# Optimization experiments

Measured on AMD Instinct MI355X. Metric: run time of the kernel, lower is better.

The kernel has to match this reference:

```python
import jax, jax.numpy as jnp
import numpy as np

N_NODES = 50000
N_EDGES = 1600000
N_FEATURES = 1433
HIDDEN = 256
N_CLASSES = 7


def setup_inputs() -> dict:
    key = jax.random.key(0)
    ks = jax.random.split(key, 5)
    x = jax.random.normal(ks[0], (N_NODES, N_FEATURES), dtype=jnp.float32)
    edge_index = jax.random.randint(ks[1], (2, N_EDGES), 0, N_NODES, dtype=jnp.int64)
    # Glorot-style init like PyG's Linear inside GCNConv
    W1 = jax.random.normal(ks[2], (N_FEATURES, HIDDEN), dtype=jnp.float32) * (1.0 / np.sqrt(N_FEATURES))
    b1 = jnp.zeros((HIDDEN,), dtype=jnp.float32)
    W2 = jax.random.normal(ks[3], (HIDDEN, N_CLASSES), dtype=jnp.float32) * (1.0 / np.sqrt(HIDDEN))
    b2 = jnp.zeros((N_CLASSES,), dtype=jnp.float32)
    return {"x": x, "edge_index": edge_index, "W1": W1, "b1": b1, "W2": W2, "b2": b2}


def _gcn_conv(x, W, b, src, dst, n_nodes):
    """PyG GCNConv: add self-loops, symmetric deg^{-1/2} norm, linear, scatter-add, +bias."""
    h = x @ W  # [N, out]
    loop = jnp.arange(n_nodes, dtype=src.dtype)
    src2 = jnp.concatenate([src, loop])
    dst2 = jnp.concatenate([dst, loop])
    ones = jnp.ones(src2.shape[0], dtype=h.dtype)
    deg = jax.ops.segment_sum(ones, dst2, num_segments=n_nodes)
    dinv = jnp.where(deg > 0, jax.lax.rsqrt(deg), 0.0)
    norm = dinv[src2] * dinv[dst2]  # [E+N]
    msg = h[src2] * norm[:, None]   # gather + scale
    out = jax.ops.segment_sum(msg, dst2, num_segments=n_nodes)
    return out + b


def reference(x, edge_index, W1, b1, W2, b2):
    src, dst = edge_index[0], edge_index[1]
    h = _gcn_conv(x, W1, b1, src, dst, N_NODES)
    h = jax.nn.relu(h)
    # dropout p=0.5 is identity in eval mode (training=False)
    out = _gcn_conv(h, W2, b2, src, dst, N_NODES)
    return out
```

## Files before the change

### kernel.cpp

```cpp
#include <hip/hip_runtime.h>
#include <hip/hip_bf16.h>


#define N_NODES_   50000
#define NB_ROWS_   50048
#define N_EDGES_   1600000
#define N_FEAT_    1433
#define K_PAD_     1440
#define HIDDEN_    256
#define N_CLASSES_ 7
#define NPART_     ((N_NODES_ + 255) / 256)
#define NT_        (K_PAD_ / 32)

typedef __attribute__((ext_vector_type(8))) short short8;
typedef __attribute__((ext_vector_type(8))) unsigned short ushort8;
typedef __attribute__((ext_vector_type(4))) float f32x4;
typedef unsigned int u32;
typedef unsigned short u16;

__device__ __forceinline__ u16 f2bf(float f) {
    __hip_bfloat16 h = __float2bfloat16(f);
    return *(u16*)&h;
}
__device__ __forceinline__ float bf2f(u16 u) {
    return __uint_as_float((u32)u << 16);
}

__global__ void deg_kernel(const int* __restrict__ dst, int* __restrict__ deg) {
    int i = blockIdx.x * blockDim.x + threadIdx.x;
    if (i < N_EDGES_) atomicAdd(&deg[dst[i]], 1);
}

__global__ void dinv_kernel(const int* __restrict__ deg, float* __restrict__ dinv) {
    int i = blockIdx.x * blockDim.x + threadIdx.x;
    if (i < N_NODES_) dinv[i] = rsqrtf((float)(deg[i] + 1));
}

__global__ __launch_bounds__(256) void scan1_kernel(const int* __restrict__ deg,
                                                    int* __restrict__ partial) {
    __shared__ int ws[4];
    int t = threadIdx.x, b = blockIdx.x;
    int idx = b * 256 + t;
    int v = (idx < N_NODES_) ? deg[idx] : 0;
    #pragma unroll
    for (int off = 32; off > 0; off >>= 1) v += __shfl_down(v, off, 64);
    if ((t & 63) == 0) ws[t >> 6] = v;
    __syncthreads();
    if (t == 0) partial[b] = ws[0] + ws[1] + ws[2] + ws[3];
}

__global__ __launch_bounds__(256) void scan2_kernel(int* __restrict__ partial,
                                                    int* __restrict__ blk_off) {
    __shared__ int sh[256];
    int t = threadIdx.x;
    int v = (t < NPART_) ? partial[t] : 0;
    sh[t] = v;
    __syncthreads();
    #pragma unroll
    for (int off = 1; off < 256; off <<= 1) {
        int a = (t >= off) ? sh[t - off] : 0;
        __syncthreads();
        sh[t] += a;
        __syncthreads();
    }
    if (t < NPART_) blk_off[t] = sh[t] - v;
}

__global__ __launch_bounds__(256) void scan3_kernel(const int* __restrict__ deg,
                                                    const int* __restrict__ blk_off,
                                                    int* __restrict__ row_ptr,
                                                    int* __restrict__ cursor) {
    __shared__ int sh[256];
    int t = threadIdx.x, b = blockIdx.x;
    int idx = b * 256 + t;
    int v = (idx < N_NODES_) ? deg[idx] : 0;
    sh[t] = v;
    __syncthreads();
    #pragma unroll
    for (int off = 1; off < 256; off <<= 1) {
        int a = (t >= off) ? sh[t - off] : 0;
        __syncthreads();
        sh[t] += a;
        __syncthreads();
    }
    if (idx < N_NODES_) {
        int rp = blk_off[b] + sh[t] - v;
        row_ptr[idx] = rp;
        cursor[idx]  = rp;
    }
    if (idx == 0) row_ptr[N_NODES_] = N_EDGES_;
}

__global__ void csr_scatter_kernel(const int* __restrict__ src, const int* __restrict__ dst,
                                   int* __restrict__ cursor, int* __restrict__ csr_src) {
    int i = blockIdx.x * blockDim.x + threadIdx.x;
    if (i >= N_EDGES_) return;
    int d = dst[i];
    int pos = atomicAdd(&cursor[d], 1);
    csr_src[pos] = src[i];
}

__global__ void w1t_kernel(const float* __restrict__ W1, u16* __restrict__ W1T) {
    int gid = blockIdx.x * blockDim.x + threadIdx.x;
    if (gid >= HIDDEN_ * K_PAD_) return;
    int k = gid % K_PAD_, n = gid / K_PAD_;
    float v = (k < N_FEAT_) ? W1[(long)k * HIDDEN_ + n] : 0.f;
    W1T[(long)n * K_PAD_ + k] = f2bf(v);
}

__global__ __launch_bounds__(256) void gemm1_fused(const float* __restrict__ X,
                                                   const u16* __restrict__ BT,
                                                   const float* __restrict__ dinv,
                                                   u16* __restrict__ C) {
    __shared__ u16 As[2 * 32 * 32];

    const int tid  = threadIdx.x;
    const int lane = tid & 63;
    const int wv   = tid >> 6;
    const int row0 = blockIdx.x * 32;

    f32x4 acc[2][4] = {};

    const int ar = tid >> 5;
    const int ak = tid & 31;
    const int awc = (ak >> 3);
    const int awo = (ak & 7);
    const int fm = lane & 15;
    const int q  = lane >> 4;

    const u16* bbase = BT + (long)(wv * 64 + fm) * K_PAD_ + q * 8;

    float av[4];

    #pragma unroll
    for (int j = 0; j < 4; j++) {
        int rcl = min(row0 + ar + 8 * j, N_NODES_ - 1);
        av[j] = X[(long)rcl * N_FEAT_ + ak];
    }
    #pragma unroll
    for (int j = 0; j < 4; j++) {
        int r = ar + 8 * j;
        As[r * 32 + ((awc ^ ((r >> 1) & 3)) << 3) + awo] = f2bf(av[j]);
    }
    __syncthreads();

    int buf = 0;
    for (int t = 0; t < NT_ - 1; ++t) {
        const int k0  = t * 32;
        const int k0n = k0 + 32;
        int kcl = min(k0n + ak, N_FEAT_ - 1);
        #pragma unroll
        for (int j = 0; j < 4; j++) {
            int rcl = min(row0 + ar + 8 * j, N_NODES_ - 1);
            av[j] = X[(long)rcl * N_FEAT_ + kcl];
        }
        short8 bfr[4];
        #pragma unroll
        for (int ni = 0; ni < 4; ni++)
            bfr[ni] = *(const short8*)(bbase + (long)ni * 16 * K_PAD_ + k0);
        short8 af[2];
        #pragma unroll
        for (int mi = 0; mi < 2; mi++) {
            int ra = mi * 16 + fm;
            af[mi] = *(const short8*)&As[buf * 1024 + ra * 32 + ((q ^ ((ra >> 1) & 3)) << 3)];
        }
        #pragma unroll
        for (int mi = 0; mi < 2; mi++)
            #pragma unroll
            for (int ni = 0; ni < 4; ni++)
                acc[mi][ni] = __builtin_amdgcn_mfma_f32_16x16x32_bf16(af[mi], bfr[ni], acc[mi][ni], 0, 0, 0);
        #pragma unroll
        for (int j = 0; j < 4; j++) {
            int r = ar + 8 * j;
            As[(buf ^ 1) * 1024 + r * 32 + ((awc ^ ((r >> 1) & 3)) << 3) + awo] = f2bf(av[j]);
        }
        __syncthreads();
        buf ^= 1;
    }

    {
        const int k0 = (NT_ - 1) * 32;
        short8 bfr[4];
        #pragma unroll
        for (int ni = 0; ni < 4; ni++)
            bfr[ni] = *(const short8*)(bbase + (long)ni * 16 * K_PAD_ + k0);
        short8 af[2];
        #pragma unroll
        for (int mi = 0; mi < 2; mi++) {
            int ra = mi * 16 + fm;
            af[mi] = *(const short8*)&As[buf * 1024 + ra * 32 + ((q ^ ((ra >> 1) & 3)) << 3)];
        }
        #pragma unroll
        for (int mi = 0; mi < 2; mi++)
            #pragma unroll
            for (int ni = 0; ni < 4; ni++)
                acc[mi][ni] = __builtin_amdgcn_mfma_f32_16x16x32_bf16(af[mi], bfr[ni], acc[mi][ni], 0, 0, 0);
    }

    const int q4 = (lane >> 4) * 4;
    #pragma unroll
    for (int mi = 0; mi < 2; mi++) {
        #pragma unroll
        for (int r = 0; r < 4; r++) {
            int gm = row0 + mi * 16 + q4 + r;
            if (gm < N_NODES_) {
                float sc = dinv[gm];
                #pragma unroll
                for (int ni = 0; ni < 4; ni++) {
                    int gn = wv * 64 + ni * 16 + fm;
                    C[(long)gm * HIDDEN_ + gn] = f2bf(acc[mi][ni][r] * sc);
                }
            }
        }
    }
}

__global__ __launch_bounds__(256) void agg_gemm2_kernel(const u16* __restrict__ h1s,
                                                        const int* __restrict__ row_ptr,
                                                        const int* __restrict__ csr_src,
                                                        const float* __restrict__ dinv,
                                                        const float* __restrict__ b1,
                                                        const float* __restrict__ W2,
                                                        float* __restrict__ h2s) {
    __shared__ float w2s[HIDDEN_ * N_CLASSES_];
    __shared__ float b1s[HIDDEN_];
    int tid = threadIdx.x;
    for (int i = tid; i < HIDDEN_ * N_CLASSES_; i += 256) w2s[i] = W2[i];
    for (int i = tid; i < HIDDEN_; i += 256) b1s[i] = b1[i];
    __syncthreads();

    int wave = tid >> 6;
    int lane = tid & 63;
    int node = blockIdx.x * 4 + wave;
    if (node >= N_NODES_) return;

    int e0 = row_ptr[node], e1 = row_ptr[node + 1];
    float ax = 0.f, ay = 0.f, az = 0.f, aw = 0.f;

    int sL = (e0 + lane < e1) ? csr_src[e0 + lane] : N_NODES_;
    for (int base = e0; base < e1; base += 64) {
        int sCur = sL;
        int nb = base + 64;
        if (nb < e1) sL = (nb + lane < e1) ? csr_src[nb + lane] : N_NODES_;
        int cnt8 = (min(64, e1 - base) + 7) & ~7;
        for (int j = 0; j < cnt8; j += 8) {
            #pragma unroll
            for (int t = 0; t < 8; t++) {
                int s = __shfl(sCur, j + t, 64);
                ushort4 u = ((const ushort4*)(h1s + (long)s * HIDDEN_))[lane];
                ax += bf2f(u.x);
                ay += bf2f(u.y);
                az += bf2f(u.z);
                aw += bf2f(u.w);
            }
        }
    }
    float nd = dinv[node];
    ushort4 su = ((const ushort4*)(h1s + (long)node * HIDDEN_))[lane];
    float xv[4];
    xv[0] = fmaxf((ax + bf2f(su.x)) * nd + b1s[lane * 4 + 0], 0.f);
    xv[1] = fmaxf((ay + bf2f(su.y)) * nd + b1s[lane * 4 + 1], 0.f);
    xv[2] = fmaxf((az + bf2f(su.z)) * nd + b1s[lane * 4 + 2], 0.f);
    xv[3] = fmaxf((aw + bf2f(su.w)) * nd + b1s[lane * 4 + 3], 0.f);

    float p[N_CLASSES_];
    #pragma unroll
    for (int c = 0; c < N_CLASSES_; c++) {
        float a = 0.f;
        #pragma unroll
        for (int i = 0; i < 4; i++)
            a += xv[i] * w2s[(lane * 4 + i) * N_CLASSES_ + c];
        p[c] = a;
    }
    #pragma unroll
    for (int off = 32; off > 0; off >>= 1)
        #pragma unroll
        for (int c = 0; c < N_CLASSES_; c++)
            p[c] += __shfl_down(p[c], off, 64);
    if (lane == 0) {
        #pragma unroll
        for (int c = 0; c < N_CLASSES_; c++)
            h2s[(long)node * 8 + c] = p[c] * nd;
    }
}

__global__ void out_kernel(const float* __restrict__ h2s,
                           const int* __restrict__ row_ptr,
                           const int* __restrict__ csr_src,
                           const float* __restrict__ dinv,
                           const float* __restrict__ b2,
                           float* __restrict__ out) {
    long gid = (long)blockIdx.x * blockDim.x + threadIdx.x;
    int node = (int)(gid >> 3);
    int c = (int)(gid & 7);
    if (node >= N_NODES_ || c >= N_CLASSES_) return;
    int e0 = row_ptr[node], e1 = row_ptr[node + 1];
    float acc = 0.f;
    for (int e = e0; e < e1; e += 4) {
        int s0 = csr_src[e];
        int s1 = (e + 1 < e1) ? csr_src[e + 1] : N_NODES_;
        int s2 = (e + 2 < e1) ? csr_src[e + 2] : N_NODES_;
        int s3 = (e + 3 < e1) ? csr_src[e + 3] : N_NODES_;
        float v0 = h2s[(long)s0 * 8 + c];
        float v1 = h2s[(long)s1 * 8 + c];
        float v2 = h2s[(long)s2 * 8 + c];
        float v3 = h2s[(long)s3 * 8 + c];
        acc += (v0 + v1) + (v2 + v3);
    }
    float nd = dinv[node];
    out[(long)node * N_CLASSES_ + c] =
        (acc + h2s[(long)node * 8 + c]) * nd + b2[c];
}

extern "C" void kernel_launch(void* const* d_in, const int* in_sizes, int n_in,
                              void* d_out, int out_size, void* d_ws, size_t ws_size,
                              hipStream_t stream) {
    const float* x   = (const float*)d_in[0];
    const int*   ei  = (const int*)d_in[1];
    const int*   src = ei;
    const int*   dst = ei + N_EDGES_;
    const float* W1  = (const float*)d_in[2];
    const float* b1  = (const float*)d_in[3];
    const float* W2  = (const float*)d_in[4];
    const float* b2  = (const float*)d_in[5];
    float* out = (float*)d_out;

    char* ws = (char*)d_ws;
    size_t off = 0;
    auto alloc = [&](size_t bytes) { void* p = ws + off; off = (off + bytes + 255) & ~(size_t)255; return p; };
    u16*   h1s     = (u16*)alloc((size_t)(N_NODES_ + 1) * HIDDEN_ * 2);
    u16*   w1t     = (u16*)alloc((size_t)HIDDEN_ * K_PAD_ * 2);
    float* h2s     = (float*)alloc((size_t)(N_NODES_ + 1) * 8 * 4);
    int*   deg     = (int*)alloc((size_t)N_NODES_ * 4);
    float* dinv    = (float*)alloc((size_t)N_NODES_ * 4);
    int*   row_ptr = (int*)alloc((size_t)(N_NODES_ + 1) * 4);
    int*   cursor  = (int*)alloc((size_t)N_NODES_ * 4);
    int*   csr_src = (int*)alloc((size_t)N_EDGES_ * 4);
    int*   partial = (int*)alloc((size_t)NPART_ * 4);
    int*   blk_off = (int*)alloc((size_t)NPART_ * 4);

    hipMemsetAsync(deg, 0, (size_t)N_NODES_ * 4, stream);
    hipMemsetAsync(h1s + (size_t)N_NODES_ * HIDDEN_, 0, HIDDEN_ * 2, stream);
    hipMemsetAsync(h2s + (size_t)N_NODES_ * 8, 0, 8 * 4, stream);

    deg_kernel<<<(N_EDGES_ + 255) / 256, 256, 0, stream>>>(dst, deg);
    dinv_kernel<<<(N_NODES_ + 255) / 256, 256, 0, stream>>>(deg, dinv);
    scan1_kernel<<<NPART_, 256, 0, stream>>>(deg, partial);
    scan2_kernel<<<1, 256, 0, stream>>>(partial, blk_off);
    scan3_kernel<<<NPART_, 256, 0, stream>>>(deg, blk_off, row_ptr, cursor);
    csr_scatter_kernel<<<(N_EDGES_ + 255) / 256, 256, 0, stream>>>(src, dst, cursor, csr_src);

    w1t_kernel<<<(HIDDEN_ * K_PAD_ + 255) / 256, 256, 0, stream>>>(W1, w1t);

    gemm1_fused<<<NB_ROWS_ / 32, 256, 0, stream>>>(x, w1t, dinv, h1s);

    agg_gemm2_kernel<<<(N_NODES_ + 3) / 4, 256, 0, stream>>>(h1s, row_ptr, csr_src, dinv, b1, W2, h2s);

    long out_threads = (long)N_NODES_ * 8;
    out_kernel<<<(unsigned)((out_threads + 255) / 256), 256, 0, stream>>>(h2s, row_ptr, csr_src, dinv, b2, out);
}
```

Baseline: 855.9 us.

## Load X fragments directly into MFMA registers, dropping LDS staging in gemm1

The first GEMM no longer stages X tiles through double-buffered shared memory with barriers. Each wave now reads its own MFMA A-fragments straight from global memory as 8 contiguous floats per lane, converts them to bf16 in registers, and prefetches the next K-step one iteration ahead. This removes the LDS writes, LDS reads and __syncthreads per K-step. The cost is that all four waves redundantly load the same X rows from global memory/L2, and lanes issue strided 32-byte row reads.

```diff
diff --git a/kernel.cpp b/kernel.cpp
--- a/kernel.cpp
+++ b/kernel.cpp
@@ -112,92 +112,69 @@
                                                    const u16* __restrict__ BT,
                                                    const float* __restrict__ dinv,
                                                    u16* __restrict__ C) {
-    __shared__ u16 As[2 * 32 * 32];
-
     const int tid  = threadIdx.x;
     const int lane = tid & 63;
     const int wv   = tid >> 6;
     const int row0 = blockIdx.x * 32;
 
-    f32x4 acc[2][4] = {};
-
-    const int ar = tid >> 5;
-    const int ak = tid & 31;
-    const int awc = (ak >> 3);
-    const int awo = (ak & 7);
     const int fm = lane & 15;
     const int q  = lane >> 4;
 
-    const u16* bbase = BT + (long)(wv * 64 + fm) * K_PAD_ + q * 8;
-
-    float av[4];
-
-    #pragma unroll
-    for (int j = 0; j < 4; j++) {
-        int rcl = min(row0 + ar + 8 * j, N_NODES_ - 1);
-        av[j] = X[(long)rcl * N_FEAT_ + ak];
-    }
-    #pragma unroll
-    for (int j = 0; j < 4; j++) {
-        int r = ar + 8 * j;
-        As[r * 32 + ((awc ^ ((r >> 1) & 3)) << 3) + awo] = f2bf(av[j]);
-    }
-    __syncthreads();
-
-    int buf = 0;
+    f32x4 acc[2][4] = {};
+
+    const int r0 = min(row0 + fm,      N_NODES_ - 1);
+    const int r1 = min(row0 + 16 + fm, N_NODES_ - 1);
+    const float* xb0 = X + (long)r0 * N_FEAT_ + q * 8;
+    const float* xb1 = X + (long)r1 * N_FEAT_ + q * 8;
+    const u16*   bb  = BT + (long)(wv * 64 + fm) * K_PAD_ + q * 8;
+
+    float  na0[8], na1[8];
+    short8 nb[4];
+    short8 af[2], bfr[4];
+
+    #pragma unroll
+    for (int j = 0; j < 8; j++) { na0[j] = xb0[j]; na1[j] = xb1[j]; }
+    #pragma unroll
+    for (int ni = 0; ni < 4; ni++)
+        nb[ni] = *(const short8*)(bb + (long)ni * 16 * K_PAD_);
+    #pragma unroll
+    for (int j = 0; j < 8; j++) { af[0][j] = (short)f2bf(na0[j]); af[1][j] = (short)f2bf(na1[j]); }
+    #pragma unroll
+    for (int ni = 0; ni < 4; ni++) bfr[ni] = nb[ni];
+
     for (int t = 0; t < NT_ - 1; ++t) {
-        const int k0  = t * 32;
-        const int k0n = k0 + 32;
-        int kcl = min(k0n + ak, N_FEAT_ - 1);
-        #pragma unroll
-        for (int j = 0; j < 4; j++) {
-            int rcl = min(row0 + ar + 8 * j, N_NODES_ - 1);
-            av[j] = X[(long)rcl * N_FEAT_ + kcl];
+        const int k0n = (t + 1) * 32;
+        if (t < NT_ - 2) {
+            #pragma unroll
+            for (int j = 0; j < 8; j++) { na0[j] = xb0[k0n + j]; na1[j] = xb1[k0n + j]; }
+        } else {
+            #pragma unroll
+            for (int j = 0; j < 8; j++) {
+                bool ok = (k0n + q * 8 + j) < N_FEAT_;
+                na0[j] = ok ? xb0[k0n + j] : 0.f;
+                na1[j] = ok ? xb1[k0n + j] : 0.f;
+            }
         }
-        short8 bfr[4];
         #pragma unroll
         for (int ni = 0; ni < 4; ni++)
-            bfr[ni] = *(const short8*)(bbase + (long)ni * 16 * K_PAD_ + k0);
-        short8 af[2];
-        #pragma unroll
-        for (int mi = 0; mi < 2; mi++) {
-            int ra = mi * 16 + fm;
-            af[mi] = *(const short8*)&As[buf * 1024 + ra * 32 + ((q ^ ((ra >> 1) & 3)) << 3)];
-        }
+            nb[ni] = *(const short8*)(bb + (long)ni * 16 * K_PAD_ + k0n);
         #pragma unroll
         for (int mi = 0; mi < 2; mi++)
             #pragma unroll
             for (int ni = 0; ni < 4; ni++)
                 acc[mi][ni] = __builtin_amdgcn_mfma_f32_16x16x32_bf16(af[mi], bfr[ni], acc[mi][ni], 0, 0, 0);
         #pragma unroll
-        for (int j = 0; j < 4; j++) {
-            int r = ar + 8 * j;
-            As[(buf ^ 1) * 1024 + r * 32 + ((awc ^ ((r >> 1) & 3)) << 3) + awo] = f2bf(av[j]);
-        }
-        __syncthreads();
-        buf ^= 1;
-    }
-
-    {
-        const int k0 = (NT_ - 1) * 32;
-        short8 bfr[4];
+        for (int j = 0; j < 8; j++) { af[0][j] = (short)f2bf(na0[j]); af[1][j] = (short)f2bf(na1[j]); }
+        #pragma unroll
+        for (int ni = 0; ni < 4; ni++) bfr[ni] = nb[ni];
+    }
+    #pragma unroll
+    for (int mi = 0; mi < 2; mi++)
         #pragma unroll
         for (int ni = 0; ni < 4; ni++)
-            bfr[ni] = *(const short8*)(bbase + (long)ni * 16 * K_PAD_ + k0);
-        short8 af[2];
-        #pragma unroll
-        for (int mi = 0; mi < 2; mi++) {
-            int ra = mi * 16 + fm;
-            af[mi] = *(const short8*)&As[buf * 1024 + ra * 32 + ((q ^ ((ra >> 1) & 3)) << 3)];
-        }
-        #pragma unroll
-        for (int mi = 0; mi < 2; mi++)
-            #pragma unroll
-            for (int ni = 0; ni < 4; ni++)
-                acc[mi][ni] = __builtin_amdgcn_mfma_f32_16x16x32_bf16(af[mi], bfr[ni], acc[mi][ni], 0, 0, 0);
-    }
-
-    const int q4 = (lane >> 4) * 4;
+            acc[mi][ni] = __builtin_amdgcn_mfma_f32_16x16x32_bf16(af[mi], bfr[ni], acc[mi][ni], 0, 0, 0);
+
+    const int q4 = q * 4;
     #pragma unroll
     for (int mi = 0; mi < 2; mi++) {
         #pragma unroll
```

Measured after the change: 905.0 us. +5.7%, slower.
